# Optimization experiments

Hardware: AMD Instinct MI355X
Metric: run time of the kernel (lower is better)

Reference implementation:

```python
import jax, jax.numpy as jnp
import numpy as np

B, LD, LE = 32, 256, 258          # batch, decoder len (split_num), encoder len (split_num+2)
ENC, DEC, HID = 512, 512, 512     # encoder_size, decoder_size(=GRU hidden), GRU hidden
MLP, NL = 256, 4                  # biaffine mlp size, num transition labels


def setup_inputs() -> dict:
    key = jax.random.key(0)
    ks = jax.random.split(key, 12)
    s = 0.05  # modest init scale for stability
    return {
        "e_outputs": jax.random.normal(ks[0], (B, LE, ENC), jnp.float32),
        "d_inputs": jax.random.normal(ks[1], (B, LD, HID), jnp.float32),
        "h0": jax.random.normal(ks[2], (B, HID), jnp.float32),
        "W_ih": jax.random.normal(ks[3], (3 * HID, HID), jnp.float32) * s,
        "W_hh": jax.random.normal(ks[4], (3 * HID, HID), jnp.float32) * s,
        "b_ih": jnp.zeros((3 * HID,), jnp.float32),
        "b_hh": jnp.zeros((3 * HID,), jnp.float32),
        "e_mlp_w": jax.random.normal(ks[5], (MLP, ENC), jnp.float32) * s,
        "e_mlp_b": jnp.zeros((MLP,), jnp.float32),
        "d_mlp_w": jax.random.normal(ks[6], (MLP, DEC), jnp.float32) * s,
        "d_mlp_b": jnp.zeros((MLP,), jnp.float32),
        "W_e": jax.random.normal(ks[7], (NL, MLP), jnp.float32) * s,
        "W_d": jax.random.normal(ks[8], (NL, MLP), jnp.float32) * s,
        "U": jax.random.normal(ks[9], (NL, MLP, MLP), jnp.float32) * s,
        "b_aff": jnp.zeros((NL, 1, 1), jnp.float32),
    }


def reference(e_outputs, d_inputs, h0, W_ih, W_hh, b_ih, b_hh,
              e_mlp_w, e_mlp_b, d_mlp_w, d_mlp_b, W_e, W_d, U, b_aff):
    def gru_step(h, x):
        gi = x @ W_ih.T + b_ih            # (B, 3H)
        gh = h @ W_hh.T + b_hh            # (B, 3H)
        i_r, i_z, i_n = jnp.split(gi, 3, axis=-1)
        h_r, h_z, h_n = jnp.split(gh, 3, axis=-1)
        r = jax.nn.sigmoid(i_r + h_r)
        z = jax.nn.sigmoid(i_z + h_z)
        n = jnp.tanh(i_n + r * h_n)
        h_new = (1.0 - z) * n + z * h
        return h_new, h_new

    xs = jnp.swapaxes(d_inputs, 0, 1)     # (LD, B, HID)
    _, hs = jax.lax.scan(gru_step, h0, xs)
    d_outputs = jnp.swapaxes(hs, 0, 1)    # (B, LD, HID)

    # --- biaffine pointer scoring (BiAffineAttention.forward) ---
    e_h = jax.nn.relu(e_outputs @ e_mlp_w.T + e_mlp_b)   # (B, LE, MLP)
    d_h = jax.nn.relu(d_outputs @ d_mlp_w.T + d_mlp_b)   # (B, LD, MLP)

    out_e = jnp.einsum('lh,beh->ble', W_e, e_h)[:, :, None, :]   # (B, NL, 1, LE)
    out_d = jnp.einsum('lh,bdh->bld', W_d, d_h)[:, :, :, None]   # (B, NL, LD, 1)
    out_u = jnp.einsum('bdh,lhk,bek->blde', d_h, U, e_h)         # (B, NL, LD, LE)

    out = out_e + out_d + out_u + b_aff                          # b_aff: (NL,1,1)
    return jnp.transpose(out, (0, 2, 3, 1))                      # (B, LD, LE, NL)
```

## Files before the change

kernel.cpp:

```cpp
#include <hip/hip_runtime.h>
#include <hip/hip_fp16.h>
#include <math.h>

#define NB   32
#define LD   256
#define LE   258
#define HID  512
#define H3   1536
#define MLP  256
#define NL   4

typedef _Float16 h2 __attribute__((ext_vector_type(2)));

__global__ void k_init(uint32_t* __restrict__ hbuf){
  int i = blockIdx.x*256 + threadIdx.x;
  if (i < 2*NB*HID) hbuf[i] = 0u;
}

__global__ __launch_bounds__(192,1)
void k_gru(const float* __restrict__ GI, const float* __restrict__ W_hh,
           const float* __restrict__ b_hh, const float* __restrict__ h0,
           float* __restrict__ dout, float* __restrict__ hbuf){
  const int wg  = blockIdx.x;
  const int b   = wg >> 3, g = wg & 7;
  const int tid = threadIdx.x;
  const int sect = tid >> 6;
  const int u    = tid & 63;
  const int c    = sect*HID + g*64 + u;

  __shared__ __align__(16) float h_lds[HID];
  __shared__ float zs[64], gs[64], ns[64];

  h2 w[256];
  const float4* wr = (const float4*)(W_hh + (size_t)c*HID);
  #pragma unroll
  for (int i=0;i<128;i++){
    float4 v = wr[i];
    h2 p0; p0[0]=(_Float16)v.x; p0[1]=(_Float16)v.y;
    h2 p1; p1[0]=(_Float16)v.z; p1[1]=(_Float16)v.w;
    w[2*i] = p0; w[2*i+1] = p1;
  }
  const float bh = b_hh[c];
  float h_old = (tid < 64) ? h0[(size_t)b*HID + g*64 + u] : 0.f;
  const float* gi_base = GI + (size_t)b*LD*H3 + c;
  float* db = dout + (size_t)b*LD*HID + g*64;

  const int w0 = tid, w1 = tid + 192, w2 = tid + 384;

  for (int i=tid;i<HID;i+=192) h_lds[i] = h0[(size_t)b*HID + i];
  __syncthreads();

  float gi = gi_base[0];
  for (int t=0;t<LD;t++){
    float a0=0.f, a1=0.f, a2=0.f, a3=0.f;
    const float4* hl = (const float4*)h_lds;
    #pragma unroll
    for (int kk=0;kk<128;kk++){
      float4 hv = hl[kk];
      h2 q0 = w[2*kk], q1 = w[2*kk+1];
      a0 = fmaf((float)q0[0], hv.x, a0);
      a1 = fmaf((float)q0[1], hv.y, a1);
      a2 = fmaf((float)q1[0], hv.z, a2);
      a3 = fmaf((float)q1[1], hv.w, a3);
    }
    float hh = (a0+a1) + (a2+a3) + bh;
    if (sect==1)      zs[u] = gi + hh;
    else if (sect==2){ gs[u] = gi; ns[u] = hh; }
    float pre_r = gi + hh;
    __syncthreads();

    if (t < LD-1){
      float gnext = gi_base[(size_t)(t+1)*H3];
      uint32_t* hb = (uint32_t*)(hbuf + (size_t)((t+1)&1)*(NB*HID) + (size_t)b*HID);
      const uint32_t want = (uint32_t)(t+1) & 7u;
      if (tid < 64){
        float r = __builtin_amdgcn_rcpf(1.f + __expf(-pre_r));
        float z = __builtin_amdgcn_rcpf(1.f + __expf(-zs[u]));
        float x = gs[u] + r*ns[u];
        float e2 = __expf(2.f*x);
        float n = 1.f - 2.f*__builtin_amdgcn_rcpf(e2 + 1.f);
        float hnew = (1.f-z)*n + z*h_old;
        h_old = hnew;
        uint32_t wb = (__builtin_bit_cast(uint32_t, hnew) & ~7u) | want;
        __hip_atomic_store(hb + g*64 + u, wb,
                           __ATOMIC_RELAXED, __HIP_MEMORY_SCOPE_AGENT);
        db[(size_t)t*HID + u] = hnew;
      }
      uint32_t* hlu = (uint32_t*)h_lds;
      bool ok = false; int guard = 0;
      while (!ok && guard < (1<<17)){
        uint32_t x0 = __hip_atomic_load(hb+w0, __ATOMIC_RELAXED, __HIP_MEMORY_SCOPE_AGENT);
        uint32_t x1 = __hip_atomic_load(hb+w1, __ATOMIC_RELAXED, __HIP_MEMORY_SCOPE_AGENT);
        uint32_t x2 = want;
        if (w2 < HID)
          x2 = __hip_atomic_load(hb+w2, __ATOMIC_RELAXED, __HIP_MEMORY_SCOPE_AGENT);
        hlu[w0] = x0; hlu[w1] = x1;
        if (w2 < HID) hlu[w2] = x2;
        ok = ((x0&7u)==want) & ((x1&7u)==want) & ((x2&7u)==want);
        if (!ok){ ++guard; __builtin_amdgcn_s_sleep(1); }
      }
      __syncthreads();
      gi = gnext;
    } else {
      if (tid < 64){
        float r = __builtin_amdgcn_rcpf(1.f + __expf(-pre_r));
        float z = __builtin_amdgcn_rcpf(1.f + __expf(-zs[u]));
        float x = gs[u] + r*ns[u];
        float e2 = __expf(2.f*x);
        float n = 1.f - 2.f*__builtin_amdgcn_rcpf(e2 + 1.f);
        float hnew = (1.f-z)*n + z*h_old;
        db[(size_t)t*HID + u] = hnew;
      }
    }
  }
}

template<int BIAS, int RELU>
__global__ __launch_bounds__(256)
void k_gemm_nt(const float* __restrict__ A, const float* __restrict__ Bm,
               const float* __restrict__ bias, float* __restrict__ C,
               int M, int N, int K){
  __shared__ float As[32][68];
  __shared__ float Bs[32][68];
  const int bm = blockIdx.y*64, bn = blockIdx.x*64;
  const int tid = threadIdx.x;
  const int tx = tid & 15, ty = tid >> 4;
  const int lr = tid >> 3;
  const int lk = (tid & 7) << 2;
  const float* A0 = A + (size_t)(bm+lr)*K + lk;
  const float* A1 = A + (size_t)(bm+lr+32)*K + lk;
  const float* B0 = Bm + (size_t)(bn+lr)*K + lk;
  const float* B1 = Bm + (size_t)(bn+lr+32)*K + lk;
  float acc[4][4] = {};
  for (int k0=0;k0<K;k0+=32){
    float4 a0 = *(const float4*)(A0 + k0);
    float4 a1 = *(const float4*)(A1 + k0);
    float4 b0 = *(const float4*)(B0 + k0);
    float4 b1 = *(const float4*)(B1 + k0);
    __syncthreads();
    As[lk+0][lr]=a0.x; As[lk+1][lr]=a0.y; As[lk+2][lr]=a0.z; As[lk+3][lr]=a0.w;
    As[lk+0][lr+32]=a1.x; As[lk+1][lr+32]=a1.y; As[lk+2][lr+32]=a1.z; As[lk+3][lr+32]=a1.w;
    Bs[lk+0][lr]=b0.x; Bs[lk+1][lr]=b0.y; Bs[lk+2][lr]=b0.z; Bs[lk+3][lr]=b0.w;
    Bs[lk+0][lr+32]=b1.x; Bs[lk+1][lr+32]=b1.y; Bs[lk+2][lr+32]=b1.z; Bs[lk+3][lr+32]=b1.w;
    __syncthreads();
    #pragma unroll
    for (int kk=0;kk<32;kk++){
      float4 av = *(const float4*)&As[kk][ty<<2];
      float4 bv = *(const float4*)&Bs[kk][tx<<2];
      float a4[4] = {av.x,av.y,av.z,av.w};
      float b4[4] = {bv.x,bv.y,bv.z,bv.w};
      #pragma unroll
      for (int i=0;i<4;i++)
        #pragma unroll
        for (int j=0;j<4;j++)
          acc[i][j] = fmaf(a4[i], b4[j], acc[i][j]);
    }
  }
  #pragma unroll
  for (int i=0;i<4;i++){
    int m = bm + (ty<<2) + i;
    #pragma unroll
    for (int j=0;j<4;j++){
      int n = bn + (tx<<2) + j;
      float v = acc[i][j];
      if (BIAS) v += bias[n];
      if (RELU) v = fmaxf(v, 0.f);
      C[(size_t)m*N + n] = v;
    }
  }
}

__global__ __launch_bounds__(256)
void k_gemm_nn_T(const float* __restrict__ A, const float* __restrict__ U,
                 float* __restrict__ T){
  __shared__ float As[32][68];
  __shared__ float Bs[32][68];
  const int l = blockIdx.z;
  const float* Bm = U + (size_t)l*MLP*MLP;
  float* C = T + (size_t)l*NB*LD*MLP;
  const int bm = blockIdx.y*64, bn = blockIdx.x*64;
  const int tid = threadIdx.x;
  const int tx = tid & 15, ty = tid >> 4;
  const int lr = tid >> 3;
  const int lk = (tid & 7) << 2;
  const int bk_r = tid >> 4;
  const int bn_c = (tid & 15) << 2;
  const float* A0 = A + (size_t)(bm+lr)*MLP + lk;
  const float* A1 = A + (size_t)(bm+lr+32)*MLP + lk;
  float acc[4][4] = {};
  for (int k0=0;k0<MLP;k0+=32){
    float4 a0 = *(const float4*)(A0 + k0);
    float4 a1 = *(const float4*)(A1 + k0);
    float4 u0 = *(const float4*)(Bm + (size_t)(k0+bk_r)*MLP + bn + bn_c);
    float4 u1 = *(const float4*)(Bm + (size_t)(k0+bk_r+16)*MLP + bn + bn_c);
    __syncthreads();
    As[lk+0][lr]=a0.x; As[lk+1][lr]=a0.y; As[lk+2][lr]=a0.z; As[lk+3][lr]=a0.w;
    As[lk+0][lr+32]=a1.x; As[lk+1][lr+32]=a1.y; As[lk+2][lr+32]=a1.z; As[lk+3][lr+32]=a1.w;
    *(float4*)&Bs[bk_r][bn_c]    = u0;
    *(float4*)&Bs[bk_r+16][bn_c] = u1;
    __syncthreads();
    #pragma unroll
    for (int kk=0;kk<32;kk++){
      float4 av = *(const float4*)&As[kk][ty<<2];
      float4 bv = *(const float4*)&Bs[kk][tx<<2];
      float a4[4] = {av.x,av.y,av.z,av.w};
      float b4[4] = {bv.x,bv.y,bv.z,bv.w};
      #pragma unroll
      for (int i=0;i<4;i++)
        #pragma unroll
        for (int j=0;j<4;j++)
          acc[i][j] = fmaf(a4[i], b4[j], acc[i][j]);
    }
  }
  #pragma unroll
  for (int i=0;i<4;i++){
    int m = bm + (ty<<2) + i;
    #pragma unroll
    for (int j=0;j<4;j++)
      C[(size_t)m*MLP + bn + (tx<<2) + j] = acc[i][j];
  }
}

__global__ void k_bilinear(const float* __restrict__ W, const float* __restrict__ Hm,
                           float* __restrict__ S, int Lrows){
  int idx = blockIdx.x*256 + threadIdx.x;
  if (idx >= NB*Lrows) return;
  int b = idx / Lrows, r = idx - b*Lrows;
  const float* row = Hm + (size_t)idx*MLP;
  float acc[NL] = {0.f,0.f,0.f,0.f};
  for (int h=0; h<MLP; h+=4){
    float4 x = *(const float4*)(row + h);
    #pragma unroll
    for (int l=0;l<NL;l++){
      float4 w = *(const float4*)(W + l*MLP + h);
      acc[l] += x.x*w.x + x.y*w.y + x.z*w.z + x.w*w.w;
    }
  }
  #pragma unroll
  for (int l=0;l<NL;l++) S[((size_t)b*NL + l)*Lrows + r] = acc[l];
}

__global__ __launch_bounds__(256)
void k_s2(const float* __restrict__ T, const float* __restrict__ eh,
          const float* __restrict__ sd, const float* __restrict__ se,
          const float* __restrict__ baff, float* __restrict__ out){
  __shared__ float As[32][68];
  __shared__ float Bs[32][68];
  const int b = blockIdx.z;
  const int d0 = blockIdx.y*64, e0 = blockIdx.x*64;
  const int tid = threadIdx.x;
  const int tx = tid & 15, ty = tid >> 4;
  const int lr = tid >> 3;
  const int lk = (tid & 7) << 2;
  const float* EH = eh + (size_t)b*LE*MLP;
  for (int l=0;l<NL;l++){
    const float* A = T + ((size_t)(l*NB + b))*LD*MLP;
    float acc[4][4] = {};
    for (int k0=0;k0<MLP;k0+=32){
      float4 a0 = *(const float4*)(A + (size_t)(d0+lr)*MLP + k0 + lk);
      float4 a1 = *(const float4*)(A + (size_t)(d0+lr+32)*MLP + k0 + lk);
      float4 z4 = make_float4(0.f,0.f,0.f,0.f);
      int er0 = e0+lr, er1 = e0+lr+32;
      float4 b0 = (er0<LE) ? *(const float4*)(EH + (size_t)er0*MLP + k0 + lk) : z4;
      float4 b1 = (er1<LE) ? *(const float4*)(EH + (size_t)er1*MLP + k0 + lk) : z4;
      __syncthreads();
      As[lk+0][lr]=a0.x; As[lk+1][lr]=a0.y; As[lk+2][lr]=a0.z; As[lk+3][lr]=a0.w;
      As[lk+0][lr+32]=a1.x; As[lk+1][lr+32]=a1.y; As[lk+2][lr+32]=a1.z; As[lk+3][lr+32]=a1.w;
      Bs[lk+0][lr]=b0.x; Bs[lk+1][lr]=b0.y; Bs[lk+2][lr]=b0.z; Bs[lk+3][lr]=b0.w;
      Bs[lk+0][lr+32]=b1.x; Bs[lk+1][lr+32]=b1.y; Bs[lk+2][lr+32]=b1.z; Bs[lk+3][lr+32]=b1.w;
      __syncthreads();
      #pragma unroll
      for (int kk=0;kk<32;kk++){
        float4 av = *(const float4*)&As[kk][ty<<2];
        float4 bv = *(const float4*)&Bs[kk][tx<<2];
        float a4[4] = {av.x,av.y,av.z,av.w};
        float b4[4] = {bv.x,bv.y,bv.z,bv.w};
        #pragma unroll
        for (int i=0;i<4;i++)
          #pragma unroll
          for (int j=0;j<4;j++)
            acc[i][j] = fmaf(a4[i], b4[j], acc[i][j]);
      }
    }
    float bl = baff[l];
    float sdl[4], sel[4];
    #pragma unroll
    for (int i=0;i<4;i++) sdl[i] = sd[((size_t)b*NL + l)*LD + d0 + (ty<<2) + i];
    #pragma unroll
    for (int j=0;j<4;j++){
      int e = e0 + (tx<<2) + j;
      sel[j] = (e<LE) ? se[((size_t)b*NL + l)*LE + e] : 0.f;
    }
    #pragma unroll
    for (int i=0;i<4;i++){
      int d = d0 + (ty<<2) + i;
      #pragma unroll
      for (int j=0;j<4;j++){
        int e = e0 + (tx<<2) + j;
        if (e < LE)
          out[(((size_t)b*LD + d)*LE + e)*NL + l] = acc[i][j] + sdl[i] + sel[j] + bl;
      }
    }
  }
}

extern "C" void kernel_launch(void* const* d_in, const int* in_sizes, int n_in,
                              void* d_out, int out_size, void* d_ws, size_t ws_size,
                              hipStream_t stream){
  const float* e_outputs = (const float*)d_in[0];
  const float* d_inputs  = (const float*)d_in[1];
  const float* h0        = (const float*)d_in[2];
  const float* W_ih      = (const float*)d_in[3];
  const float* W_hh      = (const float*)d_in[4];
  const float* b_ih      = (const float*)d_in[5];
  const float* b_hh      = (const float*)d_in[6];
  const float* e_mlp_w   = (const float*)d_in[7];
  const float* e_mlp_b   = (const float*)d_in[8];
  const float* d_mlp_w   = (const float*)d_in[9];
  const float* d_mlp_b   = (const float*)d_in[10];
  const float* W_e       = (const float*)d_in[11];
  const float* W_d       = (const float*)d_in[12];
  const float* U         = (const float*)d_in[13];
  const float* b_aff     = (const float*)d_in[14];
  float* out = (float*)d_out;
  float* ws  = (float*)d_ws;

  float* GI   = ws;
  float* T    = ws;
  float* hbuf = ws + 12582912;
  float* dout = ws   + 12582912 + 786432;
  float* eh   = dout + 4194304;
  float* dh   = eh   + 2113536;
  float* se   = dh   + 2097152;
  float* sd   = se   + 33024;

  k_init<<<dim3((2*NB*HID+255)/256), 256, 0, stream>>>((uint32_t*)hbuf);
  k_gemm_nt<1,0><<<dim3(H3/64, (NB*LD)/64), 256, 0, stream>>>(d_inputs, W_ih, b_ih, GI, NB*LD, H3, HID);
  k_gemm_nt<1,1><<<dim3(MLP/64, (NB*LE)/64), 256, 0, stream>>>(e_outputs, e_mlp_w, e_mlp_b, eh, NB*LE, MLP, HID);
  k_gru<<<dim3(NB*8), 192, 0, stream>>>(GI, W_hh, b_hh, h0, dout, hbuf);
  k_gemm_nt<1,1><<<dim3(MLP/64, (NB*LD)/64), 256, 0, stream>>>(dout, d_mlp_w, d_mlp_b, dh, NB*LD, MLP, HID);
  k_gemm_nn_T<<<dim3(MLP/64, (NB*LD)/64, NL), 256, 0, stream>>>(dh, U, T);
  k_bilinear<<<dim3((NB*LE+255)/256), 256, 0, stream>>>(W_e, eh, se, LE);
  k_bilinear<<<dim3((NB*LD+255)/256), 256, 0, stream>>>(W_d, dh, sd, LD);
  k_s2<<<dim3(5, LD/64, NB), 256, 0, stream>>>(T, eh, sd, se, b_aff, out);
}
```

Before: 2.518 ms.

## Poll GRU hidden-state exchange through L2-local buffer with periodic device-scope fallback

The per-step cross-workgroup hidden-state exchange in the GRU recurrence now writes each value twice: a volatile store to an L2-local buffer and an agent-scope atomic store to a second buffer. Readers poll mostly with an sc0 inline-asm load, falling back to the atomic buffer every fourth iteration. Each word is now retired independently once its tag matches, and the tag is widened to 8 bits. The workgroup-to-(batch, group) mapping is permuted, which likely changes which XCD each group lands on, and the next-step GI prefetch is moved after the store. The intent is to cut spin-wait latency on the serial 256-step recurrence, at the cost of more stores and reliance on cache-coherence behaviour that could be fragile across XCDs.

```diff
diff --git a/kernel.cpp b/kernel.cpp
--- a/kernel.cpp
+++ b/kernel.cpp
@@ -12,17 +12,27 @@
 
 typedef _Float16 h2 __attribute__((ext_vector_type(2)));
 
-__global__ void k_init(uint32_t* __restrict__ hbuf){
+__device__ __forceinline__ uint32_t load_l2(const uint32_t* p){
+  uint32_t v;
+  asm volatile("global_load_dword %0, %1, off sc0\n\t"
+               "s_waitcnt vmcnt(0)"
+               : "=&v"(v) : "v"(p) : "memory");
+  return v;
+}
+
+__global__ void k_init(uint32_t* __restrict__ hb){
   int i = blockIdx.x*256 + threadIdx.x;
-  if (i < 2*NB*HID) hbuf[i] = 0u;
+  if (i < 4*NB*HID) hb[i] = 0u;
 }
 
 __global__ __launch_bounds__(192,1)
 void k_gru(const float* __restrict__ GI, const float* __restrict__ W_hh,
            const float* __restrict__ b_hh, const float* __restrict__ h0,
-           float* __restrict__ dout, float* __restrict__ hbuf){
+           float* __restrict__ dout,
+           uint32_t* __restrict__ hbufL,
+           uint32_t* __restrict__ hbufG){
   const int wg  = blockIdx.x;
-  const int b   = wg >> 3, g = wg & 7;
+  const int b   = wg & 31, g = wg >> 5;
   const int tid = threadIdx.x;
   const int sect = tid >> 6;
   const int u    = tid & 63;
@@ -70,9 +80,9 @@
     __syncthreads();
 
     if (t < LD-1){
-      float gnext = gi_base[(size_t)(t+1)*H3];
-      uint32_t* hb = (uint32_t*)(hbuf + (size_t)((t+1)&1)*(NB*HID) + (size_t)b*HID);
-      const uint32_t want = (uint32_t)(t+1) & 7u;
+      uint32_t* hbL = hbufL + (size_t)((t+1)&1)*(NB*HID) + (size_t)b*HID;
+      uint32_t* hbG = hbufG + (size_t)((t+1)&1)*(NB*HID) + (size_t)b*HID;
+      const uint32_t want = (uint32_t)(t+1) & 0xFFu;
       if (tid < 64){
         float r = __builtin_amdgcn_rcpf(1.f + __expf(-pre_r));
         float z = __builtin_amdgcn_rcpf(1.f + __expf(-zs[u]));
@@ -81,23 +91,34 @@
         float n = 1.f - 2.f*__builtin_amdgcn_rcpf(e2 + 1.f);
         float hnew = (1.f-z)*n + z*h_old;
         h_old = hnew;
-        uint32_t wb = (__builtin_bit_cast(uint32_t, hnew) & ~7u) | want;
-        __hip_atomic_store(hb + g*64 + u, wb,
+        uint32_t wb = (__builtin_bit_cast(uint32_t, hnew) & ~0xFFu) | want;
+        *(volatile uint32_t*)(hbL + g*64 + u) = wb;
+        __hip_atomic_store(hbG + g*64 + u, wb,
                            __ATOMIC_RELAXED, __HIP_MEMORY_SCOPE_AGENT);
         db[(size_t)t*HID + u] = hnew;
       }
+      float gnext = gi_base[(size_t)(t+1)*H3];
       uint32_t* hlu = (uint32_t*)h_lds;
-      bool ok = false; int guard = 0;
-      while (!ok && guard < (1<<17)){
-        uint32_t x0 = __hip_atomic_load(hb+w0, __ATOMIC_RELAXED, __HIP_MEMORY_SCOPE_AGENT);
-        uint32_t x1 = __hip_atomic_load(hb+w1, __ATOMIC_RELAXED, __HIP_MEMORY_SCOPE_AGENT);
-        uint32_t x2 = want;
-        if (w2 < HID)
-          x2 = __hip_atomic_load(hb+w2, __ATOMIC_RELAXED, __HIP_MEMORY_SCOPE_AGENT);
-        hlu[w0] = x0; hlu[w1] = x1;
-        if (w2 < HID) hlu[w2] = x2;
-        ok = ((x0&7u)==want) & ((x1&7u)==want) & ((x2&7u)==want);
-        if (!ok){ ++guard; __builtin_amdgcn_s_sleep(1); }
+      bool n0 = true, n1 = true, n2 = (w2 < HID);
+      int it = 0;
+      while ((n0 | n1 | n2) && it < (1<<20)){
+        const bool useG = ((it & 3) == 3);
+        if (n0){
+          uint32_t x = useG ? __hip_atomic_load(hbG+w0, __ATOMIC_RELAXED, __HIP_MEMORY_SCOPE_AGENT)
+                            : load_l2(hbL+w0);
+          if ((x & 0xFFu) == want){ hlu[w0] = x; n0 = false; }
+        }
+        if (n1){
+          uint32_t x = useG ? __hip_atomic_load(hbG+w1, __ATOMIC_RELAXED, __HIP_MEMORY_SCOPE_AGENT)
+                            : load_l2(hbL+w1);
+          if ((x & 0xFFu) == want){ hlu[w1] = x; n1 = false; }
+        }
+        if (n2){
+          uint32_t x = useG ? __hip_atomic_load(hbG+w2, __ATOMIC_RELAXED, __HIP_MEMORY_SCOPE_AGENT)
+                            : load_l2(hbL+w2);
+          if ((x & 0xFFu) == want){ hlu[w2] = x; n2 = false; }
+        }
+        ++it;
       }
       __syncthreads();
       gi = gnext;
@@ -327,17 +348,18 @@
 
   float* GI   = ws;
   float* T    = ws;
-  float* hbuf = ws + 12582912;
+  uint32_t* hbufL = (uint32_t*)(ws + 12582912);
+  uint32_t* hbufG = hbufL + 2*NB*HID;
   float* dout = ws   + 12582912 + 786432;
   float* eh   = dout + 4194304;
   float* dh   = eh   + 2113536;
   float* se   = dh   + 2097152;
   float* sd   = se   + 33024;
 
-  k_init<<<dim3((2*NB*HID+255)/256), 256, 0, stream>>>((uint32_t*)hbuf);
+  k_init<<<dim3((4*NB*HID+255)/256), 256, 0, stream>>>(hbufL);
   k_gemm_nt<1,0><<<dim3(H3/64, (NB*LD)/64), 256, 0, stream>>>(d_inputs, W_ih, b_ih, GI, NB*LD, H3, HID);
   k_gemm_nt<1,1><<<dim3(MLP/64, (NB*LE)/64), 256, 0, stream>>>(e_outputs, e_mlp_w, e_mlp_b, eh, NB*LE, MLP, HID);
-  k_gru<<<dim3(NB*8), 192, 0, stream>>>(GI, W_hh, b_hh, h0, dout, hbuf);
+  k_gru<<<dim3(NB*8), 192, 0, stream>>>(GI, W_hh, b_hh, h0, dout, hbufL, hbufG);
   k_gemm_nt<1,1><<<dim3(MLP/64, (NB*LD)/64), 256, 0, stream>>>(dout, d_mlp_w, d_mlp_b, dh, NB*LD, MLP, HID);
   k_gemm_nn_T<<<dim3(MLP/64, (NB*LD)/64, NL), 256, 0, stream>>>(dh, U, T);
   k_bilinear<<<dim3((NB*LE+255)/256), 256, 0, stream>>>(W_e, eh, se, LE);
```

Result: slower. 2.739 ms (+8.8%).
